# Kernel optimization log

Measured on AMD Instinct MI355X. Metric: run time of the kernel, lower is better.

Reference implementation:

```python
import jax, jax.numpy as jnp
import numpy as np

BINS = 16

def gcn_conv(x, src, tgt, W, b, n):
    # PyG GCNConv: x' = D^{-1/2}(A+I)D^{-1/2} (x W) + b, aggregate at target nodes
    h = x @ W
    loop = jnp.arange(n)
    src = jnp.concatenate([src, loop])
    tgt = jnp.concatenate([tgt, loop])
    deg = jax.ops.segment_sum(jnp.ones_like(tgt, dtype=h.dtype), tgt, num_segments=n)
    dinv = jnp.where(deg > 0, deg ** -0.5, 0.0)
    norm = dinv[src] * dinv[tgt]
    out = jax.ops.segment_sum(norm[:, None] * h[src], tgt, num_segments=n)
    return out + b

def conv_pass(x, ei, gp):
    W1, b1, W2, b2, W3, b3 = gp
    n = x.shape[0]
    src, tgt = ei[0], ei[1]
    h = jax.nn.relu(gcn_conv(x, src, tgt, W1, b1, n))
    h = jax.nn.relu(gcn_conv(h, src, tgt, W2, b2, n))
    return gcn_conv(h, src, tgt, W3, b3, n)

def attention_pool(x, Wa):
    ctx = jnp.tanh(jnp.mean(x @ Wa, axis=0))   # [d] global context
    att = jax.nn.sigmoid(x @ ctx)              # [N]
    return (x.T @ att)[:, None]                # [d,1]

def ntn(f1, f2, Wt, V, bt):
    scoring = jnp.einsum('di,dek,ej->kj', f1, Wt, f2)  # [K,1] bilinear
    block = V @ jnp.concatenate([f1, f2], axis=0)      # [K,1]
    return jax.nn.relu(scoring + block + bt)

def histogram(af1, af2):
    # torch.histc over detached similarity matrix, data-dependent min/max range
    s = jax.lax.stop_gradient(af1 @ af2.T).reshape(-1)
    mn, mx = s.min(), s.max()
    width = jnp.where(mx > mn, mx - mn, jnp.ones((), s.dtype))
    idx = jnp.clip(((s - mn) / width * BINS).astype(jnp.int32), 0, BINS - 1)
    hist = jax.ops.segment_sum(jnp.ones_like(s), idx, num_segments=BINS)
    return (hist / hist.sum())[None, :]


def reference(edge_index_1, edge_index_2, features_1, features_2, avg_v,
              W1, b1, W2, b2, W3, b3, Wa, Wt, V, bt,
              fc1_W, fc1_b, fc2_W, fc2_b, fc3_W, fc3_b, sc_W, sc_b):
    gp = (W1, b1, W2, b2, W3, b3)
    af1 = conv_pass(features_1, edge_index_1, gp)
    af2 = conv_pass(features_2, edge_index_2, gp)
    p1 = attention_pool(af1, Wa)
    p2 = attention_pool(af2, Wa)
    scores = ntn(p1, p2, Wt, V, bt).T               # [1,K]
    hist = histogram(af1, af2)                      # [1,BINS]
    scores = jnp.concatenate([scores, hist], axis=1)
    h = jax.nn.relu(scores @ fc1_W + fc1_b)
    h = jax.nn.relu(h @ fc2_W + fc2_b)
    h = jax.nn.relu(h @ fc3_W + fc3_b)
    score = jax.nn.sigmoid(h @ sc_W + sc_b).reshape(-1)  # [1]
    pre_ged = -jnp.log(score) * avg_v
    return (score, pre_ged)


def setup_inputs() -> dict:
    key = jax.random.key(0)
    ks = jax.random.split(key, 24)
    N, E, L = 8192, 262144, 64
    F1, F2, F3, K = 128, 64, 32, 16
    R1, R2, R3 = 16, 8, 4
    feat = K + BINS
    def p(i, shape, scale=0.05):
        return jax.random.normal(ks[i], shape, dtype=jnp.float32) * scale
    return {
        'edge_index_1': jax.random.randint(ks[0], (2, E), 0, N),
        'edge_index_2': jax.random.randint(ks[1], (2, E), 0, N),
        'features_1': jax.random.uniform(ks[2], (N, L), dtype=jnp.float32),
        'features_2': jax.random.uniform(ks[3], (N, L), dtype=jnp.float32),
        'avg_v': jnp.float32(10.0),
        'W1': p(4, (L, F1)), 'b1': p(5, (F1,)),
        'W2': p(6, (F1, F2)), 'b2': p(7, (F2,)),
        'W3': p(8, (F2, F3)), 'b3': p(9, (F3,)),
        'Wa': p(10, (F3, F3)),
        'Wt': p(11, (F3, F3, K)), 'V': p(12, (K, 2 * F3)), 'bt': p(13, (K, 1)),
        'fc1_W': p(14, (feat, R1)), 'fc1_b': p(15, (R1,)),
        'fc2_W': p(16, (R1, R2)), 'fc2_b': p(17, (R2,)),
        'fc3_W': p(18, (R2, R3)), 'fc3_b': p(19, (R3,)),
        'sc_W': p(20, (R3, 1)), 'sc_b': p(21, (1,)),
    }
```

## Files before the change

### kernel.cpp

```cpp
#include <hip/hip_runtime.h>
#include <math.h>


#define SIM_CHUNK 2
#define GS_PAD 16
#define GS_REP 8

using bf16x8 = __attribute__((ext_vector_type(8))) short;
using f32x4  = __attribute__((ext_vector_type(4))) float;

__device__ __forceinline__ unsigned short f2bf(float f) {
    unsigned u = __float_as_uint(f);
    unsigned r = ((u >> 16) & 1u) + 0x7FFFu;
    return (unsigned short)((u + r) >> 16);
}
__device__ __forceinline__ void bf4_load(const unsigned short* __restrict__ p,
                                         float f[4]) {
    uint2 u = *(const uint2*)p;
    f[0] = __uint_as_float(u.x << 16);
    f[1] = __uint_as_float(u.x & 0xFFFF0000u);
    f[2] = __uint_as_float(u.y << 16);
    f[3] = __uint_as_float(u.y & 0xFFFF0000u);
}
__device__ __forceinline__ uint2 bf4_pack(float a, float b, float c, float d) {
    uint2 u;
    u.x = (unsigned)f2bf(a) | ((unsigned)f2bf(b) << 16);
    u.y = (unsigned)f2bf(c) | ((unsigned)f2bf(d) << 16);
    return u;
}

template <int F>
__device__ __forceinline__ float4 aggRowBF(const unsigned short* __restrict__ hp,
                                           const int* __restrict__ offs,
                                           const int* __restrict__ esrc,
                                           int r, int fq) {
    float f[4];
    bf4_load(&hp[(size_t)r * F + fq], f);
    float ax = f[0], ay = f[1], az = f[2], aw = f[3];
    int e = offs[r], e1 = offs[r + 1];
    for (; e + 4 <= e1; e += 4) {
        int s0 = esrc[e], s1 = esrc[e + 1], s2 = esrc[e + 2], s3 = esrc[e + 3];
        float f0[4], f1[4], f2[4], f3[4];
        bf4_load(&hp[(size_t)s0 * F + fq], f0);
        bf4_load(&hp[(size_t)s1 * F + fq], f1);
        bf4_load(&hp[(size_t)s2 * F + fq], f2);
        bf4_load(&hp[(size_t)s3 * F + fq], f3);
        ax += f0[0] + f1[0]; ay += f0[1] + f1[1];
        az += f0[2] + f1[2]; aw += f0[3] + f1[3];
        ax += f2[0] + f3[0]; ay += f2[1] + f3[1];
        az += f2[2] + f3[2]; aw += f2[3] + f3[3];
    }
    for (; e < e1; ++e) {
        int s = esrc[e];
        float fs[4];
        bf4_load(&hp[(size_t)s * F + fq], fs);
        ax += fs[0]; ay += fs[1]; az += fs[2]; aw += fs[3];
    }
    return make_float4(ax, ay, az, aw);
}

__global__ void zero_ws(float4* __restrict__ p, int n4) {
    int i = blockIdx.x * 256 + threadIdx.x;
    if (i < n4) p[i] = make_float4(0.f, 0.f, 0.f, 0.f);
}

__global__ void count_tgt(const int* __restrict__ t0, const int* __restrict__ t1,
                          int* __restrict__ cnt, int N, int E) {
    int g = blockIdx.y;
    const int* t = g ? t1 : t0;
    int i = blockIdx.x * 256 + threadIdx.x;
    if (i < E) atomicAdd(&cnt[g * N + t[i]], 1);
}

__global__ __launch_bounds__(1024) void scan_offsets(const int* __restrict__ cnt_,
                                                     int* __restrict__ offs_,
                                                     int* __restrict__ cursor_,
                                                     float* __restrict__ dinv_, int N) {
    int g = blockIdx.x;
    const int* cnt = cnt_ + g * N;
    int* offs = offs_ + g * (N + 1);
    int* cursor = cursor_ + g * N;
    float* dinv = dinv_ + g * N;
    int tid = threadIdx.x, lane = tid & 63, wid = tid >> 6;
    int chunk = (N + 1023) >> 10;
    int base = tid * chunk;
    int s = 0;
    for (int i = 0; i < chunk; ++i) {
        int idx = base + i;
        if (idx < N) s += cnt[idx];
    }
    int v = s;
#pragma unroll
    for (int d = 1; d < 64; d <<= 1) {
        int u = __shfl_up(v, d);
        if (lane >= d) v += u;
    }
    __shared__ int wtot[16], wbase[16];
    if (lane == 63) wtot[wid] = v;
    __syncthreads();
    if (tid == 0) {
        int r = 0;
        for (int i = 0; i < 16; ++i) { wbase[i] = r; r += wtot[i]; }
        offs[N] = r;
    }
    __syncthreads();
    int run = wbase[wid] + (v - s);
    for (int i = 0; i < chunk; ++i) {
        int idx = base + i;
        if (idx < N) {
            int c = cnt[idx];
            offs[idx] = run;
            cursor[idx] = run;
            dinv[idx] = 1.0f / sqrtf((float)(c + 1));
            run += c;
        }
    }
}

__global__ void scatter_src(const int* __restrict__ s0, const int* __restrict__ s1,
                            const int* __restrict__ t0, const int* __restrict__ t1,
                            int* __restrict__ cursor, int* __restrict__ esrc, int N, int E) {
    int g = blockIdx.y;
    const int* src = g ? s1 : s0;
    const int* tgt = g ? t1 : t0;
    int i = blockIdx.x * 256 + threadIdx.x;
    if (i < E) {
        int t = tgt[i];
        int pos = atomicAdd(&cursor[g * N + t], 1);
        esrc[g * E + pos] = src[i];
    }
}

__global__ void xscale(const float* __restrict__ x1, const float* __restrict__ x2,
                       const float* __restrict__ dinv, unsigned short* __restrict__ xs,
                       int N) {
    int i = blockIdx.x * 256 + threadIdx.x;
    if (i >= 2 * N * 16) return;
    int row = i >> 4;
    int g = row >= N;
    const float* x = g ? x2 : x1;
    int r = row - (g ? N : 0);
    float4 v = ((const float4*)x)[(size_t)r * 16 + (i & 15)];
    float d = dinv[row];
    ((uint2*)xs)[i] = bf4_pack(d * v.x, d * v.y, d * v.z, d * v.w);
}

__global__ __launch_bounds__(256) void fusedA(const unsigned short* __restrict__ xs,
                                              const float* __restrict__ W1,
                                              const float* __restrict__ b1,
                                              const float* __restrict__ W2,
                                              unsigned short* __restrict__ t1,
                                              const int* __restrict__ offs_,
                                              const int* __restrict__ esrc_,
                                              const float* __restrict__ dinv_,
                                              int N, int E) {
    __shared__ float X[16][68];
    __shared__ float H1[16][132];
    int g = blockIdx.y;
    const unsigned short* xp = xs + (size_t)(g ? N : 0) * 64;
    const int* offs = offs_ + g * (N + 1);
    const int* esrc = esrc_ + (size_t)g * E;
    const float* dinv = dinv_ + g * N;
    int rb = blockIdx.x * 16;
    int tid = threadIdx.x;
    int tc = tid & 15, tr = tid >> 4;
    float dt_row = dinv[rb + tr];
    {
        int fq = tc * 4;
        float4 v = aggRowBF<64>(xp, offs, esrc, rb + tr, fq);
        *(float4*)&X[tr][fq] =
            make_float4(dt_row * v.x, dt_row * v.y, dt_row * v.z, dt_row * v.w);
    }
    __syncthreads();
    {
        float acc[8];
        float4 b0 = *(const float4*)&b1[tc * 8];
        float4 b4 = *(const float4*)&b1[tc * 8 + 4];
        acc[0] = b0.x; acc[1] = b0.y; acc[2] = b0.z; acc[3] = b0.w;
        acc[4] = b4.x; acc[5] = b4.y; acc[6] = b4.z; acc[7] = b4.w;
#pragma unroll 8
        for (int k = 0; k < 64; ++k) {
            float a = X[tr][k];
            float4 w0 = *(const float4*)&W1[k * 128 + tc * 8];
            float4 w4 = *(const float4*)&W1[k * 128 + tc * 8 + 4];
            acc[0] = fmaf(a, w0.x, acc[0]); acc[1] = fmaf(a, w0.y, acc[1]);
            acc[2] = fmaf(a, w0.z, acc[2]); acc[3] = fmaf(a, w0.w, acc[3]);
            acc[4] = fmaf(a, w4.x, acc[4]); acc[5] = fmaf(a, w4.y, acc[5]);
            acc[6] = fmaf(a, w4.z, acc[6]); acc[7] = fmaf(a, w4.w, acc[7]);
        }
        float4 o0, o4;
        o0.x = fmaxf(acc[0], 0.f); o0.y = fmaxf(acc[1], 0.f);
        o0.z = fmaxf(acc[2], 0.f); o0.w = fmaxf(acc[3], 0.f);
        o4.x = fmaxf(acc[4], 0.f); o4.y = fmaxf(acc[5], 0.f);
        o4.z = fmaxf(acc[6], 0.f); o4.w = fmaxf(acc[7], 0.f);
        *(float4*)&H1[tr][tc * 8] = o0;
        *(float4*)&H1[tr][tc * 8 + 4] = o4;
    }
    __syncthreads();
    {
        float acc[4] = {0.f, 0.f, 0.f, 0.f};
#pragma unroll 8
        for (int k = 0; k < 128; ++k) {
            float a = H1[tr][k];
            float4 w = *(const float4*)&W2[k * 64 + tc * 4];
            acc[0] = fmaf(a, w.x, acc[0]);
            acc[1] = fmaf(a, w.y, acc[1]);
            acc[2] = fmaf(a, w.z, acc[2]);
            acc[3] = fmaf(a, w.w, acc[3]);
        }
        size_t row = (size_t)(g ? N : 0) + rb + tr;
        *(uint2*)&t1[row * 64 + tc * 4] = bf4_pack(
            dt_row * acc[0], dt_row * acc[1], dt_row * acc[2], dt_row * acc[3]);
    }
}

__global__ __launch_bounds__(256) void fusedB(const unsigned short* __restrict__ t1,
                                              const float* __restrict__ b2,
                                              const float* __restrict__ W3,
                                              unsigned short* __restrict__ t3,
                                              const int* __restrict__ offs_,
                                              const int* __restrict__ esrc_,
                                              const float* __restrict__ dinv_,
                                              int N, int E) {
    __shared__ float X[16][68];
    int g = blockIdx.y;
    const unsigned short* hp = t1 + (size_t)(g ? N : 0) * 64;
    const int* offs = offs_ + g * (N + 1);
    const int* esrc = esrc_ + (size_t)g * E;
    const float* dinv = dinv_ + g * N;
    int rb = blockIdx.x * 16;
    int tid = threadIdx.x;
    int tc = tid & 15, tr = tid >> 4;
    float dt_row = dinv[rb + tr];
    {
        int fq = tc * 4;
        float4 bb = *(const float4*)&b2[fq];
        float4 v = aggRowBF<64>(hp, offs, esrc, rb + tr, fq);
        v.x = fmaxf(fmaf(dt_row, v.x, bb.x), 0.f);
        v.y = fmaxf(fmaf(dt_row, v.y, bb.y), 0.f);
        v.z = fmaxf(fmaf(dt_row, v.z, bb.z), 0.f);
        v.w = fmaxf(fmaf(dt_row, v.w, bb.w), 0.f);
        *(float4*)&X[tr][fq] = v;
    }
    __syncthreads();
    {
        float acc[2] = {0.f, 0.f};
#pragma unroll 8
        for (int k = 0; k < 64; ++k) {
            float a = X[tr][k];
            float2 w = *(const float2*)&W3[k * 32 + tc * 2];
            acc[0] = fmaf(a, w.x, acc[0]);
            acc[1] = fmaf(a, w.y, acc[1]);
        }
        size_t row = (size_t)(g ? N : 0) + rb + tr;
        unsigned pk = (unsigned)f2bf(dt_row * acc[0]) |
                      ((unsigned)f2bf(dt_row * acc[1]) << 16);
        *(unsigned*)&t3[row * 32 + tc * 2] = pk;
    }
}

__global__ __launch_bounds__(256) void agg3_pool(const unsigned short* __restrict__ t3,
                                                 const int* __restrict__ offs_,
                                                 const int* __restrict__ esrc_,
                                                 const float* __restrict__ dinv_,
                                                 const float* __restrict__ b,
                                                 float* __restrict__ out,
                                                 unsigned short* __restrict__ outbf,
                                                 float* __restrict__ gsum, int N, int E) {
    int g = blockIdx.y;
    const unsigned short* hp = t3 + (size_t)(g ? N : 0) * 32;
    const int* offs = offs_ + g * (N + 1);
    const int* esrc = esrc_ + (size_t)g * E;
    const float* dinv = dinv_ + g * N;
    int fq = (threadIdx.x & 7) * 4;
    int t = blockIdx.x * 32 + threadIdx.x / 8;
    float dt_row = dinv[t];
    float4 v = aggRowBF<32>(hp, offs, esrc, t, fq);
    float4 bb = *(const float4*)&b[fq];
    v.x = fmaf(dt_row, v.x, bb.x); v.y = fmaf(dt_row, v.y, bb.y);
    v.z = fmaf(dt_row, v.z, bb.z); v.w = fmaf(dt_row, v.w, bb.w);
    *(float4*)&out[((size_t)(g * N + t)) * 32 + fq] = v;
    unsigned short r4[4] = {f2bf(v.x), f2bf(v.y), f2bf(v.z), f2bf(v.w)};
    *(uint2*)&outbf[((size_t)(g * N + t)) * 32 + fq] = *(uint2*)r4;
    __shared__ float ls[32];
    if (threadIdx.x < 32) ls[threadIdx.x] = 0.f;
    __syncthreads();
    atomicAdd(&ls[fq + 0], v.x);
    atomicAdd(&ls[fq + 1], v.y);
    atomicAdd(&ls[fq + 2], v.z);
    atomicAdd(&ls[fq + 3], v.w);
    __syncthreads();
    if (threadIdx.x < 32) {
        int rep = blockIdx.x & (GS_REP - 1);
        atomicAdd(&gsum[((g * GS_REP + rep) * 32 + threadIdx.x) * GS_PAD],
                  ls[threadIdx.x]);
    }
}

__global__ __launch_bounds__(256) void simA(const unsigned short* __restrict__ afbf,
                                            const float* __restrict__ af,
                                            const float* __restrict__ gsum,
                                            const float* __restrict__ Wa,
                                            float* __restrict__ p12,
                                            float2* __restrict__ pbmm, int N, int NSIM) {
    int bid = blockIdx.x;
    int tid = threadIdx.x;
    int lane = tid & 63, wv = tid >> 6;
    if (bid >= NSIM) {
        int pb = bid - NSIM;
        int npg = N / 256;
        int g = pb / npg;
        int r = (pb % npg) * 256 + tid;
        const float* afg = af + (size_t)g * N * 32;
        __shared__ float cm[32], ctxs[32];
        if (tid < 32) {
            float s = 0.f;
#pragma unroll
            for (int rep = 0; rep < GS_REP; ++rep)
                s += gsum[((g * GS_REP + rep) * 32 + tid) * GS_PAD];
            cm[tid] = s / (float)N;
        }
        __syncthreads();
        if (tid < 32) {
            float s = 0.f;
            for (int d = 0; d < 32; ++d) s = fmaf(cm[d], Wa[d * 32 + tid], s);
            ctxs[tid] = tanhf(s);
        }
        __syncthreads();
        float rowv[32];
        const float4* row = (const float4*)(afg + (size_t)r * 32);
        float dot = 0.f;
#pragma unroll
        for (int q = 0; q < 8; ++q) {
            float4 v = row[q];
            rowv[q * 4 + 0] = v.x; rowv[q * 4 + 1] = v.y;
            rowv[q * 4 + 2] = v.z; rowv[q * 4 + 3] = v.w;
            dot = fmaf(v.x, ctxs[q * 4 + 0], dot);
            dot = fmaf(v.y, ctxs[q * 4 + 1], dot);
            dot = fmaf(v.z, ctxs[q * 4 + 2], dot);
            dot = fmaf(v.w, ctxs[q * 4 + 3], dot);
        }
        float att = 1.f / (1.f + expf(-dot));
        __shared__ float wsum[4][32];
#pragma unroll
        for (int f = 0; f < 32; ++f) {
            float v = att * rowv[f];
#pragma unroll
            for (int off = 1; off < 64; off <<= 1) v += __shfl_xor(v, off);
            if (lane == 0) wsum[wv][f] = v;
        }
        __syncthreads();
        if (tid < 32) {
            float s = wsum[0][tid] + wsum[1][tid] + wsum[2][tid] + wsum[3][tid];
            atomicAdd(&p12[g * 32 + tid], s);
        }
        return;
    }
    const unsigned short* a1 = afbf;
    const unsigned short* a2 = afbf + (size_t)N * 32;
    int nb = N >> 7;
    int nchunk = nb / SIM_CHUNK;
    int by = bid / nchunk;
    int ch = bid % nchunk;
    int r16 = lane & 15, kg = (lane >> 4) << 3;
    const unsigned short* arow = a1 + ((size_t)(by * 128 + (wv >> 1) * 64 + r16)) * 32 + kg;
    bf16x8 afr[4];
#pragma unroll
    for (int m = 0; m < 4; ++m) afr[m] = *(const bf16x8*)(arow + m * 16 * 32);
    float mn = 1e30f, mx = -1e30f;
#pragma unroll
    for (int t = 0; t < SIM_CHUNK; ++t) {
        int bx = ch * SIM_CHUNK + t;
        const unsigned short* brow =
            a2 + ((size_t)(bx * 128 + (wv & 1) * 64 + r16)) * 32 + kg;
        bf16x8 bfr[4];
#pragma unroll
        for (int n = 0; n < 4; ++n) bfr[n] = *(const bf16x8*)(brow + n * 16 * 32);
        f32x4 zero = {0.f, 0.f, 0.f, 0.f};
        f32x4 acc[4][4];
#pragma unroll
        for (int m = 0; m < 4; ++m)
#pragma unroll
            for (int n = 0; n < 4; ++n)
                acc[m][n] =
                    __builtin_amdgcn_mfma_f32_16x16x32_bf16(afr[m], bfr[n], zero, 0, 0, 0);
#pragma unroll
        for (int m = 0; m < 4; ++m)
#pragma unroll
            for (int n = 0; n < 4; ++n)
#pragma unroll
                for (int e = 0; e < 4; ++e) {
                    float v = acc[m][n][e];
                    mn = fminf(mn, v);
                    mx = fmaxf(mx, v);
                }
    }
#pragma unroll
    for (int off = 1; off < 64; off <<= 1) {
        mn = fminf(mn, __shfl_xor(mn, off));
        mx = fmaxf(mx, __shfl_xor(mx, off));
    }
    __shared__ float wmn[4], wmx[4];
    if (lane == 0) { wmn[wv] = mn; wmx[wv] = mx; }
    __syncthreads();
    if (tid == 0) {
        float bmn = fminf(fminf(wmn[0], wmn[1]), fminf(wmn[2], wmn[3]));
        float bmx = fmaxf(fmaxf(wmx[0], wmx[1]), fmaxf(wmx[2], wmx[3]));
        pbmm[bid] = make_float2(bmn, bmx);
    }
}

__global__ __launch_bounds__(256) void simB(const unsigned short* __restrict__ a1,
                                            const unsigned short* __restrict__ a2,
                                            int N, int nblk,
                                            const float2* __restrict__ pbmm,
                                            unsigned* __restrict__ pbhist) {
    int nb = N >> 7;
    int nchunk = nb / SIM_CHUNK;
    int by = blockIdx.x / nchunk;
    int ch = blockIdx.x % nchunk;
    int w = threadIdx.x >> 6, lane = threadIdx.x & 63;
    int r16 = lane & 15, kg = (lane >> 4) << 3;
    __shared__ unsigned hs[16];
    __shared__ float mnmx[2];
    if (threadIdx.x < 16) hs[threadIdx.x] = 0;
    {
        float mn2 = 1e30f, mx2 = -1e30f;
        for (int i = threadIdx.x; i < nblk; i += 256) {
            float2 vv = pbmm[i];
            mn2 = fminf(mn2, vv.x);
            mx2 = fmaxf(mx2, vv.y);
        }
#pragma unroll
        for (int off = 1; off < 64; off <<= 1) {
            mn2 = fminf(mn2, __shfl_xor(mn2, off));
            mx2 = fmaxf(mx2, __shfl_xor(mx2, off));
        }
        __shared__ float wmn2[4], wmx2[4];
        if (lane == 0) { wmn2[w] = mn2; wmx2[w] = mx2; }
        __syncthreads();
        if (threadIdx.x == 0) {
            mnmx[0] = fminf(fminf(wmn2[0], wmn2[1]), fminf(wmn2[2], wmn2[3]));
            mnmx[1] = fmaxf(fmaxf(wmx2[0], wmx2[1]), fmaxf(wmx2[2], wmx2[3]));
        }
        __syncthreads();
    }
    float mnv = mnmx[0], mxv = mnmx[1];
    float width = (mxv > mnv) ? (mxv - mnv) : 1.0f;
    float scale = 16.0f / width;
    float nbias = -mnv * scale;
    const unsigned short* arow = a1 + ((size_t)(by * 128 + (w >> 1) * 64 + r16)) * 32 + kg;
    bf16x8 afr[4];
#pragma unroll
    for (int m = 0; m < 4; ++m) afr[m] = *(const bf16x8*)(arow + m * 16 * 32);
    unsigned h4_0 = 0, h4_1 = 0, h4_2 = 0, h4_3 = 0;
#pragma unroll
    for (int t = 0; t < SIM_CHUNK; ++t) {
        int bx = ch * SIM_CHUNK + t;
        const unsigned short* brow = a2 + ((size_t)(bx * 128 + (w & 1) * 64 + r16)) * 32 + kg;
        bf16x8 bfr[4];
#pragma unroll
        for (int n = 0; n < 4; ++n) bfr[n] = *(const bf16x8*)(brow + n * 16 * 32);
        f32x4 zero = {0.f, 0.f, 0.f, 0.f};
        f32x4 acc[4][4];
#pragma unroll
        for (int m = 0; m < 4; ++m)
#pragma unroll
            for (int n = 0; n < 4; ++n)
                acc[m][n] =
                    __builtin_amdgcn_mfma_f32_16x16x32_bf16(afr[m], bfr[n], zero, 0, 0, 0);
#pragma unroll
        for (int m = 0; m < 4; ++m)
#pragma unroll
            for (int n = 0; n < 4; ++n)
#pragma unroll
                for (int e = 0; e < 4; ++e) {
                    float v = acc[m][n][e];
                    int bin = (int)fmaf(v, scale, nbias);
                    bin = bin < 0 ? 0 : (bin > 15 ? 15 : bin);
                    unsigned wbit = 1u << ((bin & 3) << 3);
                    int hi = bin >> 2;
                    h4_0 += (hi == 0) ? wbit : 0u;
                    h4_1 += (hi == 1) ? wbit : 0u;
                    h4_2 += (hi == 2) ? wbit : 0u;
                    h4_3 += (hi == 3) ? wbit : 0u;
                }
    }
    unsigned hh[8];
    hh[0] = h4_0 & 0x00FF00FFu; hh[1] = (h4_0 >> 8) & 0x00FF00FFu;
    hh[2] = h4_1 & 0x00FF00FFu; hh[3] = (h4_1 >> 8) & 0x00FF00FFu;
    hh[4] = h4_2 & 0x00FF00FFu; hh[5] = (h4_2 >> 8) & 0x00FF00FFu;
    hh[6] = h4_3 & 0x00FF00FFu; hh[7] = (h4_3 >> 8) & 0x00FF00FFu;
#pragma unroll
    for (int off = 1; off < 64; off <<= 1) {
#pragma unroll
        for (int q = 0; q < 8; ++q) hh[q] += (unsigned)__shfl_xor((int)hh[q], off);
    }
    __syncthreads();
    if (lane < 16) {
        int q = lane >> 2, r = lane & 3;
        unsigned word = hh[2 * q + (r & 1)];
        unsigned val = (r < 2) ? (word & 0xFFFFu) : (word >> 16);
        atomicAdd(&hs[lane], val);
    }
    __syncthreads();
    if (threadIdx.x < 16)
        pbhist[(size_t)blockIdx.x * 16 + threadIdx.x] = hs[threadIdx.x];
}

__global__ __launch_bounds__(256) void ntn_final(
    const float* __restrict__ p12, const float* __restrict__ Wt,
    const float* __restrict__ V, const float* __restrict__ bt,
    const unsigned* __restrict__ pbhist, int nblk,
    const float* __restrict__ fc1W, const float* __restrict__ fc1b,
    const float* __restrict__ fc2W, const float* __restrict__ fc2b,
    const float* __restrict__ fc3W, const float* __restrict__ fc3b,
    const float* __restrict__ scW, const float* __restrict__ scb,
    const float* __restrict__ avg_v, float* __restrict__ out) {
    __shared__ float p1l[32], p2l[32];
    __shared__ float scp[16][17];
    __shared__ unsigned hs[16];
    __shared__ float sc[16];
    __shared__ float sfeat[32];
    __shared__ float h1s[16];
    int t = threadIdx.x;
    if (t < 16) hs[t] = 0;
    if (t < 32) p1l[t] = p12[t];
    else if (t < 64) p2l[t - 32] = p12[t];
    __syncthreads();
    {
        const uint4* pb = (const uint4*)pbhist;
        int total = nblk * 4;
        uint4 a = {0u, 0u, 0u, 0u};
        for (int i = t; i < total; i += 256) {
            uint4 v = pb[i];
            a.x += v.x; a.y += v.y; a.z += v.z; a.w += v.w;
        }
#pragma unroll
        for (int off = 4; off < 64; off <<= 1) {
            a.x += (unsigned)__shfl_xor((int)a.x, off);
            a.y += (unsigned)__shfl_xor((int)a.y, off);
            a.z += (unsigned)__shfl_xor((int)a.z, off);
            a.w += (unsigned)__shfl_xor((int)a.w, off);
        }
        int lane = t & 63;
        if (lane < 4) {
            atomicAdd(&hs[lane * 4 + 0], a.x);
            atomicAdd(&hs[lane * 4 + 1], a.y);
            atomicAdd(&hs[lane * 4 + 2], a.z);
            atomicAdd(&hs[lane * 4 + 3], a.w);
        }
    }
    {
        int k = t & 15, dp = t >> 4;
        float s = 0.f;
#pragma unroll
        for (int dd = 0; dd < 2; ++dd) {
            int d = dp * 2 + dd;
            float a = p1l[d];
            for (int e = 0; e < 32; ++e)
                s = fmaf(a * p2l[e], Wt[(d * 32 + e) * 16 + k], s);
        }
        scp[dp][k] = s;
    }
    __syncthreads();
    if (t < 16) {
        float s = 0.f;
#pragma unroll
        for (int dp = 0; dp < 16; ++dp) s += scp[dp][t];
        float bl = 0.f;
        for (int m = 0; m < 32; ++m) bl = fmaf(V[t * 64 + m], p1l[m], bl);
        for (int m = 0; m < 32; ++m) bl = fmaf(V[t * 64 + 32 + m], p2l[m], bl);
        sc[t] = fmaxf(s + bl + bt[t], 0.f);
    }
    __syncthreads();
    if (t < 16) sfeat[t] = sc[t];
    if (t == 16) {
        unsigned tot = 0;
        for (int b = 0; b < 16; ++b) tot += hs[b];
        float ftot = (float)tot;
        for (int b = 0; b < 16; ++b) sfeat[16 + b] = (float)hs[b] / ftot;
    }
    __syncthreads();
    if (t < 16) {
        float a = fc1b[t];
        for (int m = 0; m < 32; ++m) a = fmaf(sfeat[m], fc1W[m * 16 + t], a);
        h1s[t] = fmaxf(a, 0.f);
    }
    __syncthreads();
    if (t != 0) return;
    float h2[8];
    for (int r = 0; r < 8; ++r) {
        float a = fc2b[r];
        for (int m = 0; m < 16; ++m) a = fmaf(h1s[m], fc2W[m * 8 + r], a);
        h2[r] = fmaxf(a, 0.f);
    }
    float h3[4];
    for (int r = 0; r < 4; ++r) {
        float a = fc3b[r];
        for (int m = 0; m < 8; ++m) a = fmaf(h2[m], fc3W[m * 4 + r], a);
        h3[r] = fmaxf(a, 0.f);
    }
    float z = scb[0];
    for (int m = 0; m < 4; ++m) z = fmaf(h3[m], scW[m], z);
    float sig = 1.f / (1.f + expf(-z));
    out[0] = sig;
    out[1] = -logf(sig) * avg_v[0];
}

extern "C" void kernel_launch(void* const* d_in, const int* in_sizes, int n_in,
                              void* d_out, int out_size, void* d_ws, size_t ws_size,
                              hipStream_t stream) {
    (void)n_in; (void)out_size; (void)ws_size;
    const int* ei1 = (const int*)d_in[0];
    const int* ei2 = (const int*)d_in[1];
    const float* feat1 = (const float*)d_in[2];
    const float* feat2 = (const float*)d_in[3];
    const float* avg_v = (const float*)d_in[4];
    const float* W1 = (const float*)d_in[5];
    const float* b1 = (const float*)d_in[6];
    const float* W2 = (const float*)d_in[7];
    const float* b2 = (const float*)d_in[8];
    const float* W3 = (const float*)d_in[9];
    const float* b3 = (const float*)d_in[10];
    const float* Wa = (const float*)d_in[11];
    const float* Wt = (const float*)d_in[12];
    const float* V = (const float*)d_in[13];
    const float* bt = (const float*)d_in[14];
    const float* fc1W = (const float*)d_in[15];
    const float* fc1b = (const float*)d_in[16];
    const float* fc2W = (const float*)d_in[17];
    const float* fc2b = (const float*)d_in[18];
    const float* fc3W = (const float*)d_in[19];
    const float* fc3b = (const float*)d_in[20];
    const float* scW = (const float*)d_in[21];
    const float* scb = (const float*)d_in[22];

    const int E = in_sizes[0] / 2;
    const int N = in_sizes[2] / 64;
    const int nb = N / 128;
    const int nchunk = nb / SIM_CHUNK;
    const int NSIM = nb * nchunk;

    char* w = (char*)d_ws;
    size_t off = 0;
    auto take = [&](size_t bytes) -> char* {
        char* p = w + off;
        off = (off + bytes + 255) & ~(size_t)255;
        return p;
    };
    float* gsum = (float*)take((size_t)2 * GS_REP * 32 * GS_PAD * 4);
    float* p12 = (float*)take(64 * 4);
    int* cnt = (int*)take((size_t)2 * N * 4);
    float* af = (float*)take((size_t)2 * N * 32 * 4);
    unsigned short* afbf = (unsigned short*)take((size_t)2 * N * 32 * 2);
    float2* pbmm = (float2*)take((size_t)NSIM * 8);
    unsigned* pbhist = (unsigned*)take((size_t)NSIM * 16 * 4);
    float* dinv = (float*)take((size_t)2 * N * 4);
    int* offs = (int*)take((size_t)2 * (N + 1) * 4);
    int* cursor = (int*)take((size_t)2 * N * 4);
    int* esrc = (int*)take((size_t)2 * E * 4);
    unsigned short* xs = (unsigned short*)take((size_t)2 * N * 64 * 2);
    unsigned short* t1 = (unsigned short*)take((size_t)2 * N * 64 * 2);
    unsigned short* t3 = (unsigned short*)take((size_t)2 * N * 32 * 2);

    size_t zbytes = ((char*)cnt + (size_t)2 * N * 4) - (char*)gsum;
    int zn4 = (int)(zbytes / 16);

    zero_ws<<<(zn4 + 255) / 256, 256, 0, stream>>>((float4*)gsum, zn4);
    count_tgt<<<dim3((E + 255) / 256, 2), 256, 0, stream>>>(ei1 + E, ei2 + E, cnt, N, E);
    scan_offsets<<<2, 1024, 0, stream>>>(cnt, offs, cursor, dinv, N);
    xscale<<<(2 * N * 16 + 255) / 256, 256, 0, stream>>>(feat1, feat2, dinv, xs, N);
    scatter_src<<<dim3((E + 255) / 256, 2), 256, 0, stream>>>(ei1, ei2, ei1 + E, ei2 + E,
                                                              cursor, esrc, N, E);

    fusedA<<<dim3(N / 16, 2), 256, 0, stream>>>(xs, W1, b1, W2, t1, offs, esrc, dinv, N, E);
    fusedB<<<dim3(N / 16, 2), 256, 0, stream>>>(t1, b2, W3, t3, offs, esrc, dinv, N, E);
    agg3_pool<<<dim3(N / 32, 2), 256, 0, stream>>>(t3, offs, esrc, dinv, b3, af, afbf,
                                                   gsum, N, E);
    simA<<<NSIM + (N / 256) * 2, 256, 0, stream>>>(afbf, af, gsum, Wa, p12, pbmm, N, NSIM);
    simB<<<NSIM, 256, 0, stream>>>(afbf, afbf + (size_t)N * 32, N, NSIM, pbmm, pbhist);
    ntn_final<<<1, 256, 0, stream>>>(p12, Wt, V, bt, pbhist, NSIM, fc1W, fc1b, fc2W, fc2b,
                                     fc3W, fc3b, scW, scb, avg_v, (float*)d_out);
}
```

Measured before the change: 226.5 us.

## Use bf16 MFMA for fusedA's two dense layers with pre-transposed bf16 weights

The two scalar-FMA matmuls in fusedA (64→128 and 128→64) become bf16 MFMA 16x16x32 instructions. W1 and W2 are converted to transposed bf16 copies by two extra blocks appended to the xscale launch, and the shared-memory staging buffers switch to bf16. This aims to cut the FMA instruction count and the per-thread global weight loads, at the cost of rounding the activations and weights to bf16 and writing t1 with scalar stores that may be less coalesced.

```diff
diff --git a/kernel.cpp b/kernel.cpp
--- a/kernel.cpp
+++ b/kernel.cpp
@@ -133,8 +133,26 @@
 
 __global__ void xscale(const float* __restrict__ x1, const float* __restrict__ x2,
                        const float* __restrict__ dinv, unsigned short* __restrict__ xs,
-                       int N) {
-    int i = blockIdx.x * 256 + threadIdx.x;
+                       const float* __restrict__ W1, const float* __restrict__ W2,
+                       unsigned short* __restrict__ W1t, unsigned short* __restrict__ W2t,
+                       int N, int nx) {
+    int b = blockIdx.x;
+    if (b >= nx) {
+        int which = b - nx;
+        if (which == 0) {
+            for (int i = threadIdx.x; i < 128 * 64; i += 256) {
+                int c = i >> 6, k = i & 63;
+                W1t[c * 64 + k] = f2bf(W1[k * 128 + c]);
+            }
+        } else {
+            for (int i = threadIdx.x; i < 64 * 128; i += 256) {
+                int c = i >> 7, k = i & 127;
+                W2t[c * 128 + k] = f2bf(W2[k * 64 + c]);
+            }
+        }
+        return;
+    }
+    int i = b * 256 + threadIdx.x;
     if (i >= 2 * N * 16) return;
     int row = i >> 4;
     int g = row >= N;
@@ -146,16 +164,17 @@
 }
 
 __global__ __launch_bounds__(256) void fusedA(const unsigned short* __restrict__ xs,
-                                              const float* __restrict__ W1,
+                                              const unsigned short* __restrict__ W1t,
                                               const float* __restrict__ b1,
-                                              const float* __restrict__ W2,
+                                              const unsigned short* __restrict__ W2t,
                                               unsigned short* __restrict__ t1,
                                               const int* __restrict__ offs_,
                                               const int* __restrict__ esrc_,
                                               const float* __restrict__ dinv_,
                                               int N, int E) {
-    __shared__ float X[16][68];
-    __shared__ float H1[16][132];
+    __shared__ unsigned short Xb[16][72];
+    __shared__ unsigned short H1b[16][136];
+    __shared__ float dtl[16];
     int g = blockIdx.y;
     const unsigned short* xp = xs + (size_t)(g ? N : 0) * 64;
     const int* offs = offs_ + g * (N + 1);
@@ -164,53 +183,60 @@
     int rb = blockIdx.x * 16;
     int tid = threadIdx.x;
     int tc = tid & 15, tr = tid >> 4;
-    float dt_row = dinv[rb + tr];
+    if (tid < 16) dtl[tid] = dinv[rb + tid];
     {
+        float dt_row = dinv[rb + tr];
         int fq = tc * 4;
         float4 v = aggRowBF<64>(xp, offs, esrc, rb + tr, fq);
-        *(float4*)&X[tr][fq] =
-            make_float4(dt_row * v.x, dt_row * v.y, dt_row * v.z, dt_row * v.w);
-    }
-    __syncthreads();
+        *(uint2*)&Xb[tr][fq] =
+            bf4_pack(dt_row * v.x, dt_row * v.y, dt_row * v.z, dt_row * v.w);
+    }
+    __syncthreads();
+
+    int lane = tid & 63, wv = tid >> 6;
+    int lr = lane & 15;
+    int kg = (lane >> 4) << 3;
+
+    bf16x8 a0 = *(const bf16x8*)&Xb[lr][kg];
+    bf16x8 a1 = *(const bf16x8*)&Xb[lr][32 + kg];
+
+    f32x4 zero = {0.f, 0.f, 0.f, 0.f};
+#pragma unroll
+    for (int t = 0; t < 2; ++t) {
+        int ct = wv + t * 4;
+        const unsigned short* wb = W1t + (size_t)(ct * 16 + lr) * 64;
+        bf16x8 b0 = *(const bf16x8*)&wb[kg];
+        bf16x8 b1f = *(const bf16x8*)&wb[32 + kg];
+        f32x4 acc = __builtin_amdgcn_mfma_f32_16x16x32_bf16(a0, b0, zero, 0, 0, 0);
+        acc = __builtin_amdgcn_mfma_f32_16x16x32_bf16(a1, b1f, acc, 0, 0, 0);
+        int col = ct * 16 + lr;
+        float bias = b1[col];
+#pragma unroll
+        for (int r = 0; r < 4; ++r) {
+            int row = (lane >> 4) * 4 + r;
+            float v = fmaxf(acc[r] + bias, 0.f);
+            H1b[row][col] = f2bf(v);
+        }
+    }
+    __syncthreads();
+
     {
-        float acc[8];
-        float4 b0 = *(const float4*)&b1[tc * 8];
-        float4 b4 = *(const float4*)&b1[tc * 8 + 4];
-        acc[0] = b0.x; acc[1] = b0.y; acc[2] = b0.z; acc[3] = b0.w;
-        acc[4] = b4.x; acc[5] = b4.y; acc[6] = b4.z; acc[7] = b4.w;
-#pragma unroll 8
-        for (int k = 0; k < 64; ++k) {
-            float a = X[tr][k];
-            float4 w0 = *(const float4*)&W1[k * 128 + tc * 8];
-            float4 w4 = *(const float4*)&W1[k * 128 + tc * 8 + 4];
-            acc[0] = fmaf(a, w0.x, acc[0]); acc[1] = fmaf(a, w0.y, acc[1]);
-            acc[2] = fmaf(a, w0.z, acc[2]); acc[3] = fmaf(a, w0.w, acc[3]);
-            acc[4] = fmaf(a, w4.x, acc[4]); acc[5] = fmaf(a, w4.y, acc[5]);
-            acc[6] = fmaf(a, w4.z, acc[6]); acc[7] = fmaf(a, w4.w, acc[7]);
-        }
-        float4 o0, o4;
-        o0.x = fmaxf(acc[0], 0.f); o0.y = fmaxf(acc[1], 0.f);
-        o0.z = fmaxf(acc[2], 0.f); o0.w = fmaxf(acc[3], 0.f);
-        o4.x = fmaxf(acc[4], 0.f); o4.y = fmaxf(acc[5], 0.f);
-        o4.z = fmaxf(acc[6], 0.f); o4.w = fmaxf(acc[7], 0.f);
-        *(float4*)&H1[tr][tc * 8] = o0;
-        *(float4*)&H1[tr][tc * 8 + 4] = o4;
-    }
-    __syncthreads();
-    {
-        float acc[4] = {0.f, 0.f, 0.f, 0.f};
-#pragma unroll 8
-        for (int k = 0; k < 128; ++k) {
-            float a = H1[tr][k];
-            float4 w = *(const float4*)&W2[k * 64 + tc * 4];
-            acc[0] = fmaf(a, w.x, acc[0]);
-            acc[1] = fmaf(a, w.y, acc[1]);
-            acc[2] = fmaf(a, w.z, acc[2]);
-            acc[3] = fmaf(a, w.w, acc[3]);
-        }
-        size_t row = (size_t)(g ? N : 0) + rb + tr;
-        *(uint2*)&t1[row * 64 + tc * 4] = bf4_pack(
-            dt_row * acc[0], dt_row * acc[1], dt_row * acc[2], dt_row * acc[3]);
+        int ct = wv;
+        const unsigned short* wb = W2t + (size_t)(ct * 16 + lr) * 128;
+        f32x4 acc = zero;
+#pragma unroll
+        for (int kb = 0; kb < 4; ++kb) {
+            bf16x8 af = *(const bf16x8*)&H1b[lr][kb * 32 + kg];
+            bf16x8 bf = *(const bf16x8*)&wb[kb * 32 + kg];
+            acc = __builtin_amdgcn_mfma_f32_16x16x32_bf16(af, bf, acc, 0, 0, 0);
+        }
+        int col = ct * 16 + lr;
+        size_t gbase = (size_t)(g ? N : 0) + rb;
+#pragma unroll
+        for (int r = 0; r < 4; ++r) {
+            int row = (lane >> 4) * 4 + r;
+            t1[(gbase + row) * 64 + col] = f2bf(dtl[row] * acc[r]);
+        }
     }
 }
 
@@ -663,6 +689,8 @@
     unsigned short* xs = (unsigned short*)take((size_t)2 * N * 64 * 2);
     unsigned short* t1 = (unsigned short*)take((size_t)2 * N * 64 * 2);
     unsigned short* t3 = (unsigned short*)take((size_t)2 * N * 32 * 2);
+    unsigned short* W1t = (unsigned short*)take(128 * 64 * 2);
+    unsigned short* W2t = (unsigned short*)take(64 * 128 * 2);
 
     size_t zbytes = ((char*)cnt + (size_t)2 * N * 4) - (char*)gsum;
     int zn4 = (int)(zbytes / 16);
@@ -670,11 +698,16 @@
     zero_ws<<<(zn4 + 255) / 256, 256, 0, stream>>>((float4*)gsum, zn4);
     count_tgt<<<dim3((E + 255) / 256, 2), 256, 0, stream>>>(ei1 + E, ei2 + E, cnt, N, E);
     scan_offsets<<<2, 1024, 0, stream>>>(cnt, offs, cursor, dinv, N);
-    xscale<<<(2 * N * 16 + 255) / 256, 256, 0, stream>>>(feat1, feat2, dinv, xs, N);
+    {
+        int nx = (2 * N * 16 + 255) / 256;
+        xscale<<<nx + 2, 256, 0, stream>>>(feat1, feat2, dinv, xs, W1, W2, W1t, W2t, N,
+                                           nx);
+    }
     scatter_src<<<dim3((E + 255) / 256, 2), 256, 0, stream>>>(ei1, ei2, ei1 + E, ei2 + E,
                                                               cursor, esrc, N, E);
 
-    fusedA<<<dim3(N / 16, 2), 256, 0, stream>>>(xs, W1, b1, W2, t1, offs, esrc, dinv, N, E);
+    fusedA<<<dim3(N / 16, 2), 256, 0, stream>>>(xs, W1t, b1, W2t, t1, offs, esrc, dinv,
+                                                N, E);
     fusedB<<<dim3(N / 16, 2), 256, 0, stream>>>(t1, b2, W3, t3, offs, esrc, dinv, N, E);
     agg3_pool<<<dim3(N / 32, 2), 256, 0, stream>>>(t3, offs, esrc, dinv, b3, af, afbf,
                                                    gsum, N, E);
```

Result: faster. 205.5 us (-9.3%).
